# Performance work log

Hardware: AMD Instinct MI355X
Metric: run time of the kernel (lower is better)

The kernel has to match this reference:

```python
import jax, jax.numpy as jnp
import numpy as np

N = 100_000   # nodes
E = 3_200_000 # edges (avg degree 32)
D = 256       # gnn width
H = 128       # mlp hidden
C = 5         # num classes


def _gcn_conv(x, W, b, src, dst, norm, n):
    # PyG GCNConv: h = x @ W^T, then symmetric-normalized scatter-add over edges
    h = x @ W.T
    msgs = norm[:, None] * h[src]                      # [E+N, out]
    out = jax.ops.segment_sum(msgs, dst, num_segments=n)
    return out + b


def setup_inputs() -> dict:
    key = jax.random.key(0)
    ks = jax.random.split(key, 8)
    x = jax.random.normal(ks[0], (N, D), dtype=jnp.float32)
    edge_index = jax.random.randint(ks[1], (2, E), 0, N, dtype=jnp.int32)
    def lin(k, out_d, in_d):
        return jax.random.normal(k, (out_d, in_d), dtype=jnp.float32) / np.sqrt(in_d).astype(np.float32)
    return {
        "x": x,
        "edge_index": edge_index,
        "W1": lin(ks[2], D, D), "b1": jnp.zeros((D,), jnp.float32),
        "W2": lin(ks[3], D, D), "b2": jnp.zeros((D,), jnp.float32),
        "Wm1": lin(ks[4], H, D), "bm1": jnp.zeros((H,), jnp.float32),
        "Wm2": lin(ks[5], C, H), "bm2": jnp.zeros((C,), jnp.float32),
    }


def reference(x, edge_index, W1, b1, W2, b2, Wm1, bm1, Wm2, bm2):
    # add self-loops (PyG GCNConv default add_self_loops=True)
    loop = jnp.arange(N, dtype=edge_index.dtype)
    src = jnp.concatenate([edge_index[0], loop])
    dst = jnp.concatenate([edge_index[1], loop])
    # symmetric normalization: deg from destination index (flow source_to_target)
    deg = jax.ops.segment_sum(jnp.ones(src.shape[0], x.dtype), dst, num_segments=N)
    dinv = jnp.where(deg > 0, jax.lax.rsqrt(deg), 0.0)
    norm = dinv[src] * dinv[dst]                       # [E+N]

    h = _gcn_conv(x, W1, b1, src, dst, norm, N)
    h = _gcn_conv(h, W2, b2, src, dst, norm, N)
    # MLP head (no activations in original module)
    h = h @ Wm1.T + bm1
    h = h @ Wm2.T + bm2
    return h
```

## Files before the change

kernel.cpp:

```cpp
#include <hip/hip_runtime.h>

#define N_NODES 100000
#define N_EDGES 3200000
#define DIM 256
#define HID 128
#define NCLS 5
#define BSH 7
#define BSZ 128
#define NBUCK 782
#define P1B 256
#define EPB 12500
#define HPKC 16

__global__ void k_zero(int* p, int n) {
    int i = blockIdx.x * 256 + threadIdx.x;
    if (i < n) p[i] = 0;
}

template<int K>
__global__ __launch_bounds__(256) void k_hp_stage(const float* __restrict__ A,
        const float* __restrict__ B, float* __restrict__ OUT)
{
    int t = threadIdx.x;
    int k0 = blockIdx.x * HPKC;
    float acc[NCLS] = {0, 0, 0, 0, 0};
    #pragma unroll
    for (int kk = 0; kk < HPKC; ++kk) {
        int k = k0 + kk;
        float b = B[k * DIM + t];
        #pragma unroll
        for (int c = 0; c < NCLS; ++c) acc[c] += A[c * K + k] * b;
    }
    #pragma unroll
    for (int c = 0; c < NCLS; ++c) unsafeAtomicAdd(&OUT[c * DIM + t], acc[c]);
}

__global__ __launch_bounds__(320) void k_hp_bias(const float* __restrict__ Wc,
        const float* __restrict__ W2c, const float* __restrict__ Wm2,
        const float* __restrict__ b1, const float* __restrict__ b2,
        const float* __restrict__ bm1, const float* __restrict__ bm2,
        float* __restrict__ bq, float* __restrict__ bc2)
{
    int c = threadIdx.x >> 6;
    int lane = threadIdx.x & 63;
    float s = 0.0f;
    for (int i = lane; i < DIM; i += 64) s += W2c[c * DIM + i] * b1[i];
    #pragma unroll
    for (int off = 32; off > 0; off >>= 1) s += __shfl_xor(s, off);
    float b = 0.0f;
    for (int k = lane; k < HID; k += 64) b += Wm2[c * HID + k] * bm1[k];
    for (int o = lane; o < DIM; o += 64) b += Wc[c * DIM + o] * b2[o];
    #pragma unroll
    for (int off = 32; off > 0; off >>= 1) b += __shfl_xor(b, off);
    if (lane == 0) { bq[c] = s; bc2[c] = bm2[c] + b; }
}

__global__ __launch_bounds__(1024) void k_p1hist(const int* __restrict__ dst,
        int* __restrict__ gcount, int* __restrict__ blockbase)
{
    __shared__ int lh[NBUCK];
    int tid = threadIdx.x;
    for (int i = tid; i < NBUCK; i += 1024) lh[i] = 0;
    __syncthreads();
    int s = blockIdx.x * EPB, e1 = s + EPB;
    for (int e = s + tid; e < e1; e += 1024) atomicAdd(&lh[dst[e] >> BSH], 1);
    __syncthreads();
    for (int i = tid; i < NBUCK; i += 1024) {
        int c = lh[i];
        blockbase[blockIdx.x * NBUCK + i] = c ? atomicAdd(&gcount[i], c) : 0;
    }
}
__global__ __launch_bounds__(1024) void k_scanb(const int* __restrict__ gcount,
        int* __restrict__ gbase)
{
    __shared__ int sdata[1024];
    int tid = threadIdx.x;
    int v = (tid < NBUCK) ? gcount[tid] : 0;
    sdata[tid] = v;
    __syncthreads();
    #pragma unroll
    for (int off = 1; off < 1024; off <<= 1) {
        int t = (tid >= off) ? sdata[tid - off] : 0;
        __syncthreads();
        sdata[tid] += t;
        __syncthreads();
    }
    if (tid < NBUCK) gbase[tid] = sdata[tid] - v;
    if (tid == 0) gbase[NBUCK] = N_EDGES;
}
__global__ __launch_bounds__(1024) void k_p1scatter(const int* __restrict__ src,
        const int* __restrict__ dst, const int* __restrict__ gbase,
        const int* __restrict__ blockbase, unsigned* __restrict__ ebuf)
{
    __shared__ int lh[NBUCK];
    int tid = threadIdx.x;
    for (int i = tid; i < NBUCK; i += 1024) lh[i] = 0;
    __syncthreads();
    int s = blockIdx.x * EPB, e1 = s + EPB;
    for (int e = s + tid; e < e1; e += 1024) {
        int d = dst[e];
        int b = d >> BSH;
        int r = atomicAdd(&lh[b], 1);
        int pos = gbase[b] + blockbase[blockIdx.x * NBUCK + b] + r;
        ebuf[pos] = ((unsigned)src[e] << 7) | (unsigned)(d & 127);
    }
}
__global__ __launch_bounds__(512) void k_p2(const unsigned* __restrict__ ebuf,
        const int* __restrict__ gbase, int* __restrict__ rowptr,
        float* __restrict__ dinv, int* __restrict__ esrc)
{
    __shared__ int c[BSZ];
    __shared__ int sdata[BSZ];
    __shared__ int cur[BSZ];
    int tid = threadIdx.x, b = blockIdx.x;
    if (tid < BSZ) c[tid] = 0;
    __syncthreads();
    int s = gbase[b], e1 = gbase[b + 1];
    for (int e = s + tid; e < e1; e += 512) atomicAdd(&c[ebuf[e] & 127u], 1);
    __syncthreads();
    int cnt = (tid < BSZ) ? c[tid] : 0;
    if (tid < BSZ) sdata[tid] = cnt;
    __syncthreads();
    #pragma unroll
    for (int off = 1; off < BSZ; off <<= 1) {
        int t = (tid >= off && tid < BSZ) ? sdata[tid - off] : 0;
        __syncthreads();
        if (tid < BSZ) sdata[tid] += t;
        __syncthreads();
    }
    if (tid < BSZ) {
        int rp = gbase[b] + sdata[tid] - cnt;
        cur[tid] = rp;
        int node = b * BSZ + tid;
        if (node < N_NODES) {
            rowptr[node] = rp;
            dinv[node] = rsqrtf((float)(cnt + 1));
        }
    }
    if (b == 0 && tid == 0) rowptr[N_NODES] = N_EDGES;
    __syncthreads();
    for (int e = s + tid; e < e1; e += 512) {
        unsigned p = ebuf[e];
        int pos = atomicAdd(&cur[p & 127u], 1);
        esrc[pos] = (int)(p >> 7);
    }
}

__global__ __launch_bounds__(256) void k_q(const float* __restrict__ x,
        const float* __restrict__ Wq, const float* __restrict__ dinv,
        float* __restrict__ qbuf)
{
    int wid = (blockIdx.x * 256 + threadIdx.x) >> 6;
    int lane = threadIdx.x & 63;
    int lane4 = lane * 4;
    int nwaves = gridDim.x * 4;
    float4 w[NCLS];
    #pragma unroll
    for (int c = 0; c < NCLS; ++c) w[c] = *(const float4*)(Wq + c * DIM + lane4);
    for (int d = wid; d < N_NODES; d += nwaves) {
        float4 xv = *(const float4*)(x + (size_t)d * DIM + lane4);
        float p[NCLS];
        #pragma unroll
        for (int c = 0; c < NCLS; ++c) {
            float s = xv.x * w[c].x + xv.y * w[c].y + xv.z * w[c].z + xv.w * w[c].w;
            #pragma unroll
            for (int off = 32; off > 0; off >>= 1) s += __shfl_xor(s, off);
            p[c] = s;
        }
        if (lane == 0) {
            float dv = dinv[d];
            #pragma unroll
            for (int c = 0; c < NCLS; ++c) qbuf[(size_t)d * 8 + c] = dv * p[c];
        }
    }
}

template<int MODE>
__global__ __launch_bounds__(256) void k_gather5(const float* __restrict__ in,
        const int* __restrict__ rowptr, const int* __restrict__ esrc,
        const float* __restrict__ dinv, const float* __restrict__ bias,
        float* __restrict__ out, int ostride)
{
    int gid = blockIdx.x * 256 + threadIdx.x;
    int d = gid >> 2, sub = gid & 3;
    if (d >= N_NODES) return;
    float acc0 = 0, acc1 = 0, acc2 = 0, acc3 = 0, acc4 = 0;
    int r0 = rowptr[d], r1 = rowptr[d + 1];
    for (int j = r0 + sub; j < r1; j += 4) {
        int s = esrc[j];
        float4 v = *(const float4*)(in + (size_t)s * 8);
        float v4 = in[(size_t)s * 8 + 4];
        acc0 += v.x; acc1 += v.y; acc2 += v.z; acc3 += v.w; acc4 += v4;
    }
    if (sub == 0) {
        float4 v = *(const float4*)(in + (size_t)d * 8);
        float v4 = in[(size_t)d * 8 + 4];
        acc0 += v.x; acc1 += v.y; acc2 += v.z; acc3 += v.w; acc4 += v4;
    }
    #pragma unroll
    for (int off = 1; off < 4; off <<= 1) {
        acc0 += __shfl_xor(acc0, off);
        acc1 += __shfl_xor(acc1, off);
        acc2 += __shfl_xor(acc2, off);
        acc3 += __shfl_xor(acc3, off);
        acc4 += __shfl_xor(acc4, off);
    }
    if (sub == 0) {
        float dv = dinv[d];
        float sc = (MODE == 1) ? dv * dv : dv;
        float bs = (MODE == 1) ? dv : 1.0f;
        out[(size_t)d * ostride + 0] = sc * acc0 + bs * bias[0];
        out[(size_t)d * ostride + 1] = sc * acc1 + bs * bias[1];
        out[(size_t)d * ostride + 2] = sc * acc2 + bs * bias[2];
        out[(size_t)d * ostride + 3] = sc * acc3 + bs * bias[3];
        out[(size_t)d * ostride + 4] = sc * acc4 + bs * bias[4];
    }
}

extern "C" void kernel_launch(void* const* d_in, const int* in_sizes, int n_in,
                              void* d_out, int out_size, void* d_ws, size_t ws_size,
                              hipStream_t stream)
{
    const float* x   = (const float*)d_in[0];
    const int*   ei  = (const int*)d_in[1];
    const float* W1  = (const float*)d_in[2];
    const float* b1  = (const float*)d_in[3];
    const float* W2  = (const float*)d_in[4];
    const float* b2  = (const float*)d_in[5];
    const float* Wm1 = (const float*)d_in[6];
    const float* bm1 = (const float*)d_in[7];
    const float* Wm2 = (const float*)d_in[8];
    const float* bm2 = (const float*)d_in[9];
    float* out = (float*)d_out;
    const int* src = ei;
    const int* dst = ei + N_EDGES;

    char* ws = (char*)d_ws;
    float* dinv   = (float*)(ws + 0x0000000);
    int* rowptr   = (int*)  (ws + 0x0080000);
    int* esrc     = (int*)  (ws + 0x0200000);
    float* hpw    = (float*)(ws + 0x0F00000);
    float* Wq     = hpw;
    float* Wc     = hpw + NCLS * DIM;
    float* W2c    = hpw + 2 * NCLS * DIM;
    float* bq     = (float*)(ws + 0x0F10000);
    float* bc2    = (float*)(ws + 0x0F11000);
    float* qbuf   = (float*)(ws + 0x1000000);
    float* tbuf   = (float*)(ws + 0x1400000);
    unsigned* ebuf = (unsigned*)(ws + 0x1800000);
    int* blockbase = (int*) (ws + 0x2600000);
    int* gcount    = (int*) (ws + 0x2700000);
    int* gbase     = (int*) (ws + 0x2702000);

    k_zero<<<(3 * NCLS * DIM + 255) / 256, 256, 0, stream>>>((int*)hpw, 3 * NCLS * DIM);
    k_hp_stage<HID><<<HID / HPKC, 256, 0, stream>>>(Wm2, Wm1, Wc);
    k_hp_stage<DIM><<<DIM / HPKC, 256, 0, stream>>>(Wc, W2, W2c);
    k_hp_bias<<<1, 320, 0, stream>>>(Wc, W2c, Wm2, b1, b2, bm1, bm2, bq, bc2);
    k_hp_stage<DIM><<<DIM / HPKC, 256, 0, stream>>>(W2c, W1, Wq);

    k_zero<<<(NBUCK + 255) / 256, 256, 0, stream>>>(gcount, NBUCK);
    k_p1hist<<<P1B, 1024, 0, stream>>>(dst, gcount, blockbase);
    k_scanb<<<1, 1024, 0, stream>>>(gcount, gbase);
    k_p1scatter<<<P1B, 1024, 0, stream>>>(src, dst, gbase, blockbase, ebuf);
    k_p2<<<NBUCK, 512, 0, stream>>>(ebuf, gbase, rowptr, dinv, esrc);

    k_q<<<2048, 256, 0, stream>>>(x, Wq, dinv, qbuf);

    const int GB = (N_NODES * 4 + 255) / 256;
    k_gather5<1><<<GB, 256, 0, stream>>>(qbuf, rowptr, esrc, dinv, bq, tbuf, 8);
    k_gather5<0><<<GB, 256, 0, stream>>>(tbuf, rowptr, esrc, dinv, bc2, out, NCLS);
}
```

Baseline: 347.6 us.

## Fuse head weight precompute and restructure edge bucketing to reuse recorded ranks

```diff
diff --git a/kernel.cpp b/kernel.cpp
--- a/kernel.cpp
+++ b/kernel.cpp
@@ -5,92 +5,64 @@
 #define DIM 256
 #define HID 128
 #define NCLS 5
-#define BSH 7
-#define BSZ 128
-#define NBUCK 782
+#define BSH 8
+#define BSZ 256
+#define NBUCK 391
 #define P1B 256
 #define EPB 12500
-#define HPKC 16
-
-__global__ void k_zero(int* p, int n) {
-    int i = blockIdx.x * 256 + threadIdx.x;
-    if (i < n) p[i] = 0;
-}
-
-template<int K>
-__global__ __launch_bounds__(256) void k_hp_stage(const float* __restrict__ A,
-        const float* __restrict__ B, float* __restrict__ OUT)
-{
-    int t = threadIdx.x;
-    int k0 = blockIdx.x * HPKC;
-    float acc[NCLS] = {0, 0, 0, 0, 0};
-    #pragma unroll
-    for (int kk = 0; kk < HPKC; ++kk) {
-        int k = k0 + kk;
-        float b = B[k * DIM + t];
+
+__global__ __launch_bounds__(1024) void k_head(const float* __restrict__ W1,
+        const float* __restrict__ W2, const float* __restrict__ b1,
+        const float* __restrict__ b2, const float* __restrict__ Wm1,
+        const float* __restrict__ bm1, const float* __restrict__ Wm2,
+        const float* __restrict__ bm2, float* __restrict__ Wq,
+        float* __restrict__ bq, float* __restrict__ bc2, int* __restrict__ gcount)
+{
+    __shared__ float Wc[NCLS][DIM];
+    __shared__ float W2c[NCLS][DIM];
+    int tid = threadIdx.x;
+    for (int i = tid; i < NBUCK; i += 1024) gcount[i] = 0;
+    for (int i = tid; i < NCLS * DIM; i += 1024) {
+        int c = i >> 8, o = i & 255;
+        float a = 0.0f;
+        for (int k = 0; k < HID; ++k) a += Wm2[c * HID + k] * Wm1[k * DIM + o];
+        Wc[c][o] = a;
+    }
+    __syncthreads();
+    for (int i = tid; i < NCLS * DIM; i += 1024) {
+        int c = i >> 8, o = i & 255;
+        float a = 0.0f;
+        for (int k = 0; k < DIM; ++k) a += Wc[c][k] * W2[k * DIM + o];
+        W2c[c][o] = a;
+    }
+    __syncthreads();
+    for (int i = tid; i < NCLS * DIM; i += 1024) {
+        int c = i >> 8, o = i & 255;
+        float a = 0.0f;
+        for (int k = 0; k < DIM; ++k) a += W2c[c][k] * W1[k * DIM + o];
+        Wq[c * DIM + o] = a;
+    }
+    int w = tid >> 6, lane = tid & 63;
+    if (w < NCLS) {
+        float s = 0.0f;
+        for (int i = lane; i < DIM; i += 64) s += W2c[w][i] * b1[i];
         #pragma unroll
-        for (int c = 0; c < NCLS; ++c) acc[c] += A[c * K + k] * b;
-    }
-    #pragma unroll
-    for (int c = 0; c < NCLS; ++c) unsafeAtomicAdd(&OUT[c * DIM + t], acc[c]);
-}
-
-__global__ __launch_bounds__(320) void k_hp_bias(const float* __restrict__ Wc,
-        const float* __restrict__ W2c, const float* __restrict__ Wm2,
-        const float* __restrict__ b1, const float* __restrict__ b2,
-        const float* __restrict__ bm1, const float* __restrict__ bm2,
-        float* __restrict__ bq, float* __restrict__ bc2)
-{
-    int c = threadIdx.x >> 6;
-    int lane = threadIdx.x & 63;
-    float s = 0.0f;
-    for (int i = lane; i < DIM; i += 64) s += W2c[c * DIM + i] * b1[i];
-    #pragma unroll
-    for (int off = 32; off > 0; off >>= 1) s += __shfl_xor(s, off);
-    float b = 0.0f;
-    for (int k = lane; k < HID; k += 64) b += Wm2[c * HID + k] * bm1[k];
-    for (int o = lane; o < DIM; o += 64) b += Wc[c * DIM + o] * b2[o];
-    #pragma unroll
-    for (int off = 32; off > 0; off >>= 1) b += __shfl_xor(b, off);
-    if (lane == 0) { bq[c] = s; bc2[c] = bm2[c] + b; }
-}
-
-__global__ __launch_bounds__(1024) void k_p1hist(const int* __restrict__ dst,
-        int* __restrict__ gcount, int* __restrict__ blockbase)
-{
-    __shared__ int lh[NBUCK];
-    int tid = threadIdx.x;
-    for (int i = tid; i < NBUCK; i += 1024) lh[i] = 0;
-    __syncthreads();
-    int s = blockIdx.x * EPB, e1 = s + EPB;
-    for (int e = s + tid; e < e1; e += 1024) atomicAdd(&lh[dst[e] >> BSH], 1);
-    __syncthreads();
-    for (int i = tid; i < NBUCK; i += 1024) {
-        int c = lh[i];
-        blockbase[blockIdx.x * NBUCK + i] = c ? atomicAdd(&gcount[i], c) : 0;
-    }
-}
-__global__ __launch_bounds__(1024) void k_scanb(const int* __restrict__ gcount,
-        int* __restrict__ gbase)
-{
-    __shared__ int sdata[1024];
-    int tid = threadIdx.x;
-    int v = (tid < NBUCK) ? gcount[tid] : 0;
-    sdata[tid] = v;
-    __syncthreads();
-    #pragma unroll
-    for (int off = 1; off < 1024; off <<= 1) {
-        int t = (tid >= off) ? sdata[tid - off] : 0;
-        __syncthreads();
-        sdata[tid] += t;
-        __syncthreads();
-    }
-    if (tid < NBUCK) gbase[tid] = sdata[tid] - v;
-    if (tid == 0) gbase[NBUCK] = N_EDGES;
-}
-__global__ __launch_bounds__(1024) void k_p1scatter(const int* __restrict__ src,
-        const int* __restrict__ dst, const int* __restrict__ gbase,
-        const int* __restrict__ blockbase, unsigned* __restrict__ ebuf)
+        for (int off = 32; off > 0; off >>= 1) s += __shfl_xor(s, off);
+        if (lane == 0) bq[w] = s;
+    } else if (w < 2 * NCLS) {
+        int c = w - NCLS;
+        float bsum = 0.0f;
+        for (int k = lane; k < HID; k += 64) bsum += Wm2[c * HID + k] * bm1[k];
+        for (int o = lane; o < DIM; o += 64) bsum += Wc[c][o] * b2[o];
+        #pragma unroll
+        for (int off = 32; off > 0; off >>= 1) bsum += __shfl_xor(bsum, off);
+        if (lane == 0) bc2[c] = bm2[c] + bsum;
+    }
+}
+
+__global__ __launch_bounds__(1024) void k_build1(const int* __restrict__ dst,
+        int* __restrict__ gcount, int* __restrict__ blockbase,
+        unsigned* __restrict__ rankb)
 {
     __shared__ int lh[NBUCK];
     int tid = threadIdx.x;
@@ -101,22 +73,60 @@
         int d = dst[e];
         int b = d >> BSH;
         int r = atomicAdd(&lh[b], 1);
-        int pos = gbase[b] + blockbase[blockIdx.x * NBUCK + b] + r;
-        ebuf[pos] = ((unsigned)src[e] << 7) | (unsigned)(d & 127);
+        rankb[e] = ((unsigned)r << 17) | ((unsigned)(d & 255) << 9) | (unsigned)b;
+    }
+    __syncthreads();
+    for (int i = tid; i < NBUCK; i += 1024) {
+        int c = lh[i];
+        blockbase[blockIdx.x * NBUCK + i] = c ? atomicAdd(&gcount[i], c) : 0;
+    }
+}
+__global__ __launch_bounds__(512) void k_scanb(const int* __restrict__ gcount,
+        int* __restrict__ gbase)
+{
+    __shared__ int sdata[512];
+    int tid = threadIdx.x;
+    int v = (tid < NBUCK) ? gcount[tid] : 0;
+    sdata[tid] = v;
+    __syncthreads();
+    #pragma unroll
+    for (int off = 1; off < 512; off <<= 1) {
+        int t = (tid >= off) ? sdata[tid - off] : 0;
+        __syncthreads();
+        sdata[tid] += t;
+        __syncthreads();
+    }
+    if (tid < NBUCK) gbase[tid] = sdata[tid] - v;
+    if (tid == 0) gbase[NBUCK] = N_EDGES;
+}
+__global__ __launch_bounds__(1024) void k_scat(const int* __restrict__ src,
+        const unsigned* __restrict__ rankb, const int* __restrict__ gbase,
+        const int* __restrict__ blockbase, unsigned* __restrict__ ebuf)
+{
+    int tid = threadIdx.x;
+    const int* bb = blockbase + blockIdx.x * NBUCK;
+    int s = blockIdx.x * EPB, e1 = s + EPB;
+    for (int e = s + tid; e < e1; e += 1024) {
+        unsigned v = rankb[e];
+        unsigned b = v & 511u;
+        int pos = gbase[b] + bb[b] + (int)(v >> 17);
+        ebuf[pos] = ((unsigned)src[e] << 8) | ((v >> 9) & 255u);
     }
 }
 __global__ __launch_bounds__(512) void k_p2(const unsigned* __restrict__ ebuf,
         const int* __restrict__ gbase, int* __restrict__ rowptr,
-        float* __restrict__ dinv, int* __restrict__ esrc)
+        float* __restrict__ dinv, unsigned* __restrict__ rank2,
+        int* __restrict__ esrc)
 {
     __shared__ int c[BSZ];
     __shared__ int sdata[BSZ];
-    __shared__ int cur[BSZ];
+    __shared__ int base[BSZ];
     int tid = threadIdx.x, b = blockIdx.x;
     if (tid < BSZ) c[tid] = 0;
     __syncthreads();
     int s = gbase[b], e1 = gbase[b + 1];
-    for (int e = s + tid; e < e1; e += 512) atomicAdd(&c[ebuf[e] & 127u], 1);
+    for (int e = s + tid; e < e1; e += 512)
+        rank2[e] = (unsigned)atomicAdd(&c[ebuf[e] & 255u], 1);
     __syncthreads();
     int cnt = (tid < BSZ) ? c[tid] : 0;
     if (tid < BSZ) sdata[tid] = cnt;
@@ -129,8 +139,8 @@
         __syncthreads();
     }
     if (tid < BSZ) {
-        int rp = gbase[b] + sdata[tid] - cnt;
-        cur[tid] = rp;
+        int rp = s + sdata[tid] - cnt;
+        base[tid] = rp;
         int node = b * BSZ + tid;
         if (node < N_NODES) {
             rowptr[node] = rp;
@@ -141,8 +151,7 @@
     __syncthreads();
     for (int e = s + tid; e < e1; e += 512) {
         unsigned p = ebuf[e];
-        int pos = atomicAdd(&cur[p & 127u], 1);
-        esrc[pos] = (int)(p >> 7);
+        esrc[base[p & 255u] + (int)rank2[e]] = (int)(p >> 8);
     }
 }
 
@@ -236,33 +245,26 @@
     const int* dst = ei + N_EDGES;
 
     char* ws = (char*)d_ws;
-    float* dinv   = (float*)(ws + 0x0000000);
-    int* rowptr   = (int*)  (ws + 0x0080000);
-    int* esrc     = (int*)  (ws + 0x0200000);
-    float* hpw    = (float*)(ws + 0x0F00000);
-    float* Wq     = hpw;
-    float* Wc     = hpw + NCLS * DIM;
-    float* W2c    = hpw + 2 * NCLS * DIM;
-    float* bq     = (float*)(ws + 0x0F10000);
-    float* bc2    = (float*)(ws + 0x0F11000);
-    float* qbuf   = (float*)(ws + 0x1000000);
-    float* tbuf   = (float*)(ws + 0x1400000);
-    unsigned* ebuf = (unsigned*)(ws + 0x1800000);
-    int* blockbase = (int*) (ws + 0x2600000);
-    int* gcount    = (int*) (ws + 0x2700000);
-    int* gbase     = (int*) (ws + 0x2702000);
-
-    k_zero<<<(3 * NCLS * DIM + 255) / 256, 256, 0, stream>>>((int*)hpw, 3 * NCLS * DIM);
-    k_hp_stage<HID><<<HID / HPKC, 256, 0, stream>>>(Wm2, Wm1, Wc);
-    k_hp_stage<DIM><<<DIM / HPKC, 256, 0, stream>>>(Wc, W2, W2c);
-    k_hp_bias<<<1, 320, 0, stream>>>(Wc, W2c, Wm2, b1, b2, bm1, bm2, bq, bc2);
-    k_hp_stage<DIM><<<DIM / HPKC, 256, 0, stream>>>(W2c, W1, Wq);
-
-    k_zero<<<(NBUCK + 255) / 256, 256, 0, stream>>>(gcount, NBUCK);
-    k_p1hist<<<P1B, 1024, 0, stream>>>(dst, gcount, blockbase);
-    k_scanb<<<1, 1024, 0, stream>>>(gcount, gbase);
-    k_p1scatter<<<P1B, 1024, 0, stream>>>(src, dst, gbase, blockbase, ebuf);
-    k_p2<<<NBUCK, 512, 0, stream>>>(ebuf, gbase, rowptr, dinv, esrc);
+    float* dinv     = (float*)   (ws + 0x0000000);
+    int* rowptr     = (int*)     (ws + 0x0080000);
+    int* esrc       = (int*)     (ws + 0x0200000);
+    float* qbuf     = (float*)   (ws + 0x1000000);
+    float* tbuf     = (float*)   (ws + 0x1400000);
+    unsigned* ebuf  = (unsigned*)(ws + 0x1800000);
+    unsigned* rankb = (unsigned*)(ws + 0x2600000);
+    int* blockbase  = (int*)     (ws + 0x3400000);
+    int* gcount     = (int*)     (ws + 0x3500000);
+    int* gbase      = (int*)     (ws + 0x3502000);
+    float* Wq       = (float*)   (ws + 0x3504000);
+    float* bq       = (float*)   (ws + 0x3510000);
+    float* bc2      = (float*)   (ws + 0x3511000);
+
+    k_head<<<1, 1024, 0, stream>>>(W1, W2, b1, b2, Wm1, bm1, Wm2, bm2, Wq, bq, bc2, gcount);
+
+    k_build1<<<P1B, 1024, 0, stream>>>(dst, gcount, blockbase, rankb);
+    k_scanb<<<1, 512, 0, stream>>>(gcount, gbase);
+    k_scat<<<P1B, 1024, 0, stream>>>(src, rankb, gbase, blockbase, ebuf);
+    k_p2<<<NBUCK, 512, 0, stream>>>(ebuf, gbase, rowptr, dinv, rankb, esrc);
 
     k_q<<<2048, 256, 0, stream>>>(x, Wq, dinv, qbuf);
 
```

After: 370.9 us. +6.7%, slower.
